# Optimization experiments

Hardware: AMD Instinct MI355X
Metric: run time of the kernel (lower is better)

Reference implementation:

```python
import jax, jax.numpy as jnp
import numpy as np

N_NODES = 50000
HIDDEN = 256
IN_DIM = 1000
OUT_DIM = 2
N_EDGES = 1600000


def gcn_conv(x, W, b, src, dst, n):
    # x: [N, Fin], W: [Fin, Fout]; src/dst already include self-loops
    h = x @ W  # [N, Fout]
    deg = jax.ops.segment_sum(jnp.ones(dst.shape, h.dtype), dst, num_segments=n)
    dinv = jnp.where(deg > 0, jax.lax.rsqrt(deg), 0.0)  # deg^{-1/2}
    norm = dinv[src] * dinv[dst]  # [E]
    out = jax.ops.segment_sum(h[src] * norm[:, None], dst, num_segments=n)
    return out + b


def setup_inputs() -> dict:
    key = jax.random.key(0)
    k1, k2, k3, k4 = jax.random.split(key, 4)
    x = jax.random.normal(k1, (N_NODES, IN_DIM), dtype=jnp.float32)
    edge_index = jax.random.randint(k2, (2, N_EDGES), 0, N_NODES, dtype=jnp.int64)
    # glorot-ish init for the two GCNConv layers
    W1 = jax.random.normal(k3, (IN_DIM, HIDDEN), dtype=jnp.float32) * (1.0 / np.sqrt(IN_DIM))
    b1 = jnp.zeros((HIDDEN,), dtype=jnp.float32)
    W2 = jax.random.normal(k4, (HIDDEN, OUT_DIM), dtype=jnp.float32) * (1.0 / np.sqrt(HIDDEN))
    b2 = jnp.zeros((OUT_DIM,), dtype=jnp.float32)
    return {"x": x, "W1": W1, "b1": b1, "W2": W2, "b2": b2, "edge_index": edge_index}


def reference(x, W1, b1, W2, b2, edge_index):
    n = x.shape[0]
    loops = jnp.arange(n, dtype=edge_index.dtype)
    src = jnp.concatenate([edge_index[0], loops])  # add self-loops (PyG gcn_norm)
    dst = jnp.concatenate([edge_index[1], loops])
    h = gcn_conv(x, W1, b1, src, dst, n)
    h = jax.nn.relu(h)
    out = gcn_conv(h, W2, b2, src, dst, n)
    return out
```

## Files before the change

### kernel.cpp

```cpp
#include <hip/hip_runtime.h>
#include <math.h>

#define N_NODES 50000
#define IN_DIM  1000
#define HIDDEN  256
#define N_EDGES 1600000
#define NBLK    196
#define NSTEP   63
#define GEMM_BLOCKS ((N_NODES + 63) / 64)
#define SCAT_BLOCKS 512

typedef short bf16x8 __attribute__((ext_vector_type(8)));
typedef float f32x16 __attribute__((ext_vector_type(16)));

__device__ __forceinline__ unsigned short f2bf_rne(float f) {
    unsigned u = __builtin_bit_cast(unsigned, f);
    unsigned r = (u + 0x7FFFu + ((u >> 16) & 1u)) >> 16;
    return (unsigned short)r;
}
__device__ __forceinline__ float bf2f(unsigned short b) {
    unsigned u = ((unsigned)b) << 16;
    return __builtin_bit_cast(float, u);
}
__device__ __forceinline__ unsigned cvt_pk_bf16(float a, float b) {
    unsigned r;
    asm("v_cvt_pk_bf16_f32 %0, %1, %2" : "=v"(r) : "v"(a), "v"(b));
    return r;
}
#define GLOAD_LDS16(gp, lp) \
    __builtin_amdgcn_global_load_lds((const __attribute__((address_space(1))) unsigned*)(gp), \
                                     (__attribute__((address_space(3))) unsigned*)(lp), 16, 0, 0)

__global__ void hist_kernel(const int* __restrict__ ei, int* __restrict__ cnt) {
    int e = blockIdx.x * blockDim.x + threadIdx.x;
    int stride = gridDim.x * blockDim.x;
    for (; e < N_EDGES; e += stride) {
        int d = ei[N_EDGES + e];
        if ((unsigned)d < N_NODES) atomicAdd(&cnt[d], 1);
    }
}

__global__ __launch_bounds__(256) void scan_sums(const int* __restrict__ cnt, int* __restrict__ bsum) {
    __shared__ int s[256];
    int t = threadIdx.x;
    int i = blockIdx.x * 256 + t;
    s[t] = (i < N_NODES) ? cnt[i] : 0;
    __syncthreads();
    #pragma unroll
    for (int off = 128; off > 0; off >>= 1) {
        if (t < off) s[t] += s[t + off];
        __syncthreads();
    }
    if (t == 0) bsum[blockIdx.x] = s[0];
}

__global__ __launch_bounds__(256) void scan_top(int* __restrict__ bsum) {
    __shared__ int s[256];
    int t = threadIdx.x;
    int v = (t < NBLK) ? bsum[t] : 0;
    s[t] = v;
    __syncthreads();
    for (int off = 1; off < 256; off <<= 1) {
        int x = (t >= off) ? s[t - off] : 0;
        __syncthreads();
        s[t] += x;
        __syncthreads();
    }
    if (t < NBLK) bsum[t] = s[t] - v;
}

__global__ __launch_bounds__(256) void scan_write(const int* __restrict__ cnt, const int* __restrict__ bsum,
                                                  int* __restrict__ rowoff, int* __restrict__ cursor,
                                                  float* __restrict__ dinv) {
    __shared__ int s[256];
    int t = threadIdx.x;
    int i = blockIdx.x * 256 + t;
    int v = (i < N_NODES) ? cnt[i] : 0;
    s[t] = v;
    __syncthreads();
    for (int off = 1; off < 256; off <<= 1) {
        int x = (t >= off) ? s[t - off] : 0;
        __syncthreads();
        s[t] += x;
        __syncthreads();
    }
    if (i < N_NODES) {
        int ro = bsum[blockIdx.x] + s[t] - v;
        rowoff[i] = ro;
        cursor[i] = ro;
        dinv[i]  = rsqrtf((float)v + 1.0f);
    }
}

__global__ __launch_bounds__(256) void wsplit_kernel(const float* __restrict__ W1,
                                                     unsigned short* __restrict__ Wp) {
    int idx = blockIdx.x * 256 + threadIdx.x;
    int c = idx >> 10, k = idx & 1023;
    float v = (k < IN_DIM) ? W1[(size_t)k * HIDDEN + c] : 0.0f;
    int ci = c >> 5;
    int step = k >> 4, kk = k & 15;
    int lane = (kk >> 3) * 32 + (c & 31);
    int j = kk & 7;
    Wp[((size_t)(step * 8 + ci) * 64 + lane) * 8 + j] = f2bf_rne(v);
}

__global__ __launch_bounds__(256, 4) void gemm_scatter_fused(const float* __restrict__ X,
                                                             const unsigned short* __restrict__ Wp,
                                                             const float* __restrict__ dinv,
                                                             unsigned short* __restrict__ G1b,
                                                             const int* __restrict__ ei,
                                                             int* __restrict__ cursor,
                                                             int* __restrict__ csr) {
    __shared__ unsigned short sA[2][1024];
    __shared__ unsigned short sB[2][4096];
    const int tid = threadIdx.x;

    if (blockIdx.x >= GEMM_BLOCKS) {
        int e = (blockIdx.x - GEMM_BLOCKS) * 256 + tid;
        int stride = SCAT_BLOCKS * 256;
        for (; e < N_EDGES; e += stride) {
            int s = ei[e];
            int d = ei[N_EDGES + e];
            if ((unsigned)d < N_NODES && (unsigned)s < N_NODES) {
                int pos = atomicAdd(&cursor[d], 1);
                csr[pos] = s;
            }
        }
        return;
    }

    const int w   = tid >> 6;
    const int l   = tid & 63;
    const int lr  = l & 31;
    const int lq  = l >> 5;
    const int R   = w >> 1;
    const int C   = w & 1;
    const int m0  = blockIdx.x * 64;

    const int rl = tid >> 2;
    const int ss = tid & 3;
    const int smt   = rl >> 5;
    const int slane = (ss >> 1) * 32 + (rl & 31);
    const int sidx  = smt * 512 + slane * 8 + (ss & 1) * 4;
    int rg = m0 + rl;
    const float* ap = X + (size_t)(rg < N_NODES ? rg : N_NODES - 1) * IN_DIM + ss * 4;
    const bool svalid_tail = (ss < 2);

    const unsigned short* bsrc = Wp + (size_t)(w * 2) * 512 + l * 8;

    f32x16 acc[4] = {};

    auto stageB = [&](int s, int buf) {
        const unsigned short* src = bsrc + (size_t)s * 4096;
        GLOAD_LDS16(src,       &sB[buf][(w * 2 + 0) * 512]);
        GLOAD_LDS16(src + 512, &sB[buf][(w * 2 + 1) * 512]);
    };
    auto cvtWriteA = [&](float4 f, int buf) {
        unsigned h0 = cvt_pk_bf16(f.x, f.y);
        unsigned h1 = cvt_pk_bf16(f.z, f.w);
        *(uint2*)&sA[buf][sidx] = make_uint2(h0, h1);
    };

    stageB(0, 0);
    cvtWriteA(*(const float4*)ap, 0);
    float4 rA = *(const float4*)(ap + 16);
    __syncthreads();

    #pragma unroll 1
    for (int s = 0; s < NSTEP; ++s) {
        const int buf = s & 1;
        if (s + 1 < NSTEP) stageB(s + 1, buf ^ 1);
        float4 rN = make_float4(0.f, 0.f, 0.f, 0.f);
        if (s + 2 < NSTEP && (s + 2 < NSTEP - 1 || svalid_tail))
            rN = *(const float4*)(ap + (size_t)(s + 2) * 16);
        if (s + 1 < NSTEP) cvtWriteA(rA, buf ^ 1);

        bf16x8 ah = *(const bf16x8*)&sA[buf][R * 512 + l * 8];
        bf16x8 b[4];
        #pragma unroll
        for (int ni = 0; ni < 4; ++ni)
            b[ni] = *(const bf16x8*)&sB[buf][(C * 4 + ni) * 512 + l * 8];
        #pragma unroll
        for (int ni = 0; ni < 4; ++ni)
            acc[ni] = __builtin_amdgcn_mfma_f32_32x32x16_bf16(ah, b[ni], acc[ni], 0, 0, 0);
        rA = rN;
        __syncthreads();
    }

    #pragma unroll
    for (int r = 0; r < 16; ++r) {
        int row = m0 + R * 32 + (r & 3) + 8 * (r >> 2) + 4 * lq;
        if (row >= N_NODES) continue;
        float dv = dinv[row];
        #pragma unroll
        for (int ni = 0; ni < 4; ++ni) {
            int slab = C * 4 + ni;
            G1b[((size_t)slab * N_NODES + row) * 32 + lr] = f2bf_rne(dv * acc[ni][r]);
        }
    }
}

__global__ __launch_bounds__(256) void aggslab_kernel(const unsigned short* __restrict__ G,
                                                      const int* __restrict__ csr,
                                                      const int* __restrict__ rowoff,
                                                      const int* __restrict__ cnt,
                                                      const float* __restrict__ dinv,
                                                      const float* __restrict__ b1,
                                                      const float* __restrict__ W2,
                                                      float* __restrict__ part) {
    const int tid  = threadIdx.x;
    const int slab = blockIdx.x & 7;
    const int nb   = blockIdx.x >> 3;
    const int wave = tid >> 6, lane = tid & 63;
    const int g    = lane >> 3, sl = lane & 7;
    const int d    = nb * 32 + wave * 8 + g;
    if (d >= N_NODES) return;
    const unsigned short* Gs = G + (size_t)slab * N_NODES * 32;
    const int co = sl * 4;
    const int c0 = slab * 32 + co;

    ushort4 sv = *(const ushort4*)&Gs[(size_t)d * 32 + co];
    float ax = bf2f(sv.x), ay = bf2f(sv.y), az = bf2f(sv.z), aw = bf2f(sv.w);
    int beg = rowoff[d], num = cnt[d];
    int end = beg + num;
    int e = beg;
    for (; e + 8 <= end; e += 8) {
        int s0 = csr[e], s1 = csr[e+1], s2 = csr[e+2], s3 = csr[e+3];
        int s4 = csr[e+4], s5 = csr[e+5], s6 = csr[e+6], s7 = csr[e+7];
        ushort4 v0 = *(const ushort4*)&Gs[(size_t)s0 * 32 + co];
        ushort4 v1 = *(const ushort4*)&Gs[(size_t)s1 * 32 + co];
        ushort4 v2 = *(const ushort4*)&Gs[(size_t)s2 * 32 + co];
        ushort4 v3 = *(const ushort4*)&Gs[(size_t)s3 * 32 + co];
        ushort4 v4 = *(const ushort4*)&Gs[(size_t)s4 * 32 + co];
        ushort4 v5 = *(const ushort4*)&Gs[(size_t)s5 * 32 + co];
        ushort4 v6 = *(const ushort4*)&Gs[(size_t)s6 * 32 + co];
        ushort4 v7 = *(const ushort4*)&Gs[(size_t)s7 * 32 + co];
        ax += bf2f(v0.x); ay += bf2f(v0.y); az += bf2f(v0.z); aw += bf2f(v0.w);
        ax += bf2f(v1.x); ay += bf2f(v1.y); az += bf2f(v1.z); aw += bf2f(v1.w);
        ax += bf2f(v2.x); ay += bf2f(v2.y); az += bf2f(v2.z); aw += bf2f(v2.w);
        ax += bf2f(v3.x); ay += bf2f(v3.y); az += bf2f(v3.z); aw += bf2f(v3.w);
        ax += bf2f(v4.x); ay += bf2f(v4.y); az += bf2f(v4.z); aw += bf2f(v4.w);
        ax += bf2f(v5.x); ay += bf2f(v5.y); az += bf2f(v5.z); aw += bf2f(v5.w);
        ax += bf2f(v6.x); ay += bf2f(v6.y); az += bf2f(v6.z); aw += bf2f(v6.w);
        ax += bf2f(v7.x); ay += bf2f(v7.y); az += bf2f(v7.z); aw += bf2f(v7.w);
    }
    for (; e < end; ++e) {
        int s = csr[e];
        ushort4 v = *(const ushort4*)&Gs[(size_t)s * 32 + co];
        ax += bf2f(v.x); ay += bf2f(v.y); az += bf2f(v.z); aw += bf2f(v.w);
    }
    float dv = dinv[d];
    float4 bb = *(const float4*)&b1[c0];
    float zx = fmaxf(dv * ax + bb.x, 0.f);
    float zy = fmaxf(dv * ay + bb.y, 0.f);
    float zz = fmaxf(dv * az + bb.z, 0.f);
    float zw = fmaxf(dv * aw + bb.w, 0.f);
    float2 w0 = *(const float2*)&W2[(c0 + 0) * 2];
    float2 w1 = *(const float2*)&W2[(c0 + 1) * 2];
    float2 w2_ = *(const float2*)&W2[(c0 + 2) * 2];
    float2 w3 = *(const float2*)&W2[(c0 + 3) * 2];
    float p0 = zx * w0.x + zy * w1.x + zz * w2_.x + zw * w3.x;
    float p1 = zx * w0.y + zy * w1.y + zz * w2_.y + zw * w3.y;
    #pragma unroll
    for (int off = 1; off < 8; off <<= 1) {
        p0 += __shfl_xor(p0, off, 64);
        p1 += __shfl_xor(p1, off, 64);
    }
    if (sl == 0)
        *(float2*)&part[((size_t)slab * N_NODES + d) * 2] = make_float2(p0, p1);
}

__global__ __launch_bounds__(256) void g2reduce_kernel(const float* __restrict__ part,
                                                       const float* __restrict__ dinv,
                                                       float* __restrict__ G2) {
    int i = blockIdx.x * 256 + threadIdx.x;
    if (i >= N_NODES) return;
    float a0 = 0.f, a1 = 0.f;
    #pragma unroll
    for (int s = 0; s < 8; ++s) {
        float2 p = *(const float2*)&part[((size_t)s * N_NODES + i) * 2];
        a0 += p.x; a1 += p.y;
    }
    float dv = dinv[i];
    G2[i * 2 + 0] = dv * a0;
    G2[i * 2 + 1] = dv * a1;
}

__global__ __launch_bounds__(256) void agg2_kernel(const float* __restrict__ G2,
                                                   const int* __restrict__ csr,
                                                   const int* __restrict__ rowoff,
                                                   const int* __restrict__ cnt,
                                                   const float* __restrict__ dinv,
                                                   const float* __restrict__ b2,
                                                   float* __restrict__ out) {
    int wave = threadIdx.x >> 6, lane = threadIdx.x & 63;
    int d = blockIdx.x * 4 + wave;
    if (d >= N_NODES) return;
    int beg = rowoff[d], num = cnt[d];
    float a0 = 0.f, a1 = 0.f;
    for (int e = lane; e < num; e += 64) {
        int s = csr[beg + e];
        float2 g = *(const float2*)&G2[s * 2];
        a0 += g.x; a1 += g.y;
    }
    #pragma unroll
    for (int off = 32; off; off >>= 1) {
        a0 += __shfl_xor(a0, off, 64);
        a1 += __shfl_xor(a1, off, 64);
    }
    if (lane == 0) {
        float2 self = *(const float2*)&G2[d * 2];
        float dv = dinv[d];
        out[d * 2 + 0] = dv * (a0 + self.x) + b2[0];
        out[d * 2 + 1] = dv * (a1 + self.y) + b2[1];
    }
}

#define OFF_CNT     0u
#define OFF_ROWOFF  262144u
#define OFF_CURSOR  524288u
#define OFF_DINV    786432u
#define OFF_BSUM    1048576u
#define OFF_CSR     1310720u
#define OFF_WP      8388608u
#define OFF_G1B     9437184u
#define OFF_G2      35651584u
#define OFF_PART    36700160u

extern "C" void kernel_launch(void* const* d_in, const int* in_sizes, int n_in,
                              void* d_out, int out_size, void* d_ws, size_t ws_size,
                              hipStream_t stream) {
    const float* x  = (const float*)d_in[0];
    const float* W1 = (const float*)d_in[1];
    const float* b1 = (const float*)d_in[2];
    const float* W2 = (const float*)d_in[3];
    const float* b2 = (const float*)d_in[4];
    const int*   ei = (const int*)d_in[5];

    char* ws = (char*)d_ws;
    int*   cnt    = (int*)  (ws + OFF_CNT);
    int*   rowoff = (int*)  (ws + OFF_ROWOFF);
    int*   cursor = (int*)  (ws + OFF_CURSOR);
    float* dinv   = (float*)(ws + OFF_DINV);
    int*   bsum   = (int*)  (ws + OFF_BSUM);
    int*   csr    = (int*)  (ws + OFF_CSR);
    unsigned short* wp  = (unsigned short*)(ws + OFF_WP);
    unsigned short* g1b = (unsigned short*)(ws + OFF_G1B);
    float* g2     = (float*)(ws + OFF_G2);
    float* part   = (float*)(ws + OFF_PART);
    float* out    = (float*)d_out;

    hipMemsetAsync(cnt, 0, N_NODES * sizeof(int), stream);
    wsplit_kernel<<<1024, 256, 0, stream>>>(W1, wp);
    hist_kernel<<<2048, 256, 0, stream>>>(ei, cnt);
    scan_sums<<<NBLK, 256, 0, stream>>>(cnt, bsum);
    scan_top<<<1, 256, 0, stream>>>(bsum);
    scan_write<<<NBLK, 256, 0, stream>>>(cnt, bsum, rowoff, cursor, dinv);

    gemm_scatter_fused<<<GEMM_BLOCKS + SCAT_BLOCKS, 256, 0, stream>>>(x, wp, dinv, g1b,
                                                                      ei, cursor, csr);

    aggslab_kernel<<<8 * ((N_NODES + 31) / 32), 256, 0, stream>>>(g1b, csr, rowoff, cnt, dinv, b1, W2, part);
    g2reduce_kernel<<<NBLK, 256, 0, stream>>>(part, dinv, g2);
    agg2_kernel<<<(N_NODES + 3) / 4, 256, 0, stream>>>(g2, csr, rowoff, cnt, dinv, b2, out);
}
```

Measured before the change: 297.3 us.

## Fuse prep kernels, partition CSR scatter by node range, replace slab reduce with atomics

Merges the W1 repack and degree histogram into one launch. The CSR scatter blocks are split into 8 groups that each handle only destinations in one node range, which localizes the cursor atomics and csr writes at the cost of each group re-reading the dst array. The separate g2 reduction kernel is dropped: aggslab atomically accumulates its partial results into a zeroed buffer, and agg2 applies dinv of each source itself. This saves a launch and the partial-buffer round trip, but adds float atomics with nondeterministic summation order and one extra memset.

```diff
diff --git a/kernel.cpp b/kernel.cpp
--- a/kernel.cpp
+++ b/kernel.cpp
@@ -9,6 +9,7 @@
 #define NSTEP   63
 #define GEMM_BLOCKS ((N_NODES + 63) / 64)
 #define SCAT_BLOCKS 512
+#define NODES_PER_PART 6250
 
 typedef short bf16x8 __attribute__((ext_vector_type(8)));
 typedef float f32x16 __attribute__((ext_vector_type(16)));
@@ -31,9 +32,24 @@
     __builtin_amdgcn_global_load_lds((const __attribute__((address_space(1))) unsigned*)(gp), \
                                      (__attribute__((address_space(3))) unsigned*)(lp), 16, 0, 0)
 
-__global__ void hist_kernel(const int* __restrict__ ei, int* __restrict__ cnt) {
-    int e = blockIdx.x * blockDim.x + threadIdx.x;
-    int stride = gridDim.x * blockDim.x;
+__global__ __launch_bounds__(256) void prep_kernel(const float* __restrict__ W1,
+                                                   unsigned short* __restrict__ Wp,
+                                                   const int* __restrict__ ei,
+                                                   int* __restrict__ cnt) {
+    const int tid = threadIdx.x;
+    if (blockIdx.x < 1024) {
+        int idx = blockIdx.x * 256 + tid;
+        int c = idx >> 10, k = idx & 1023;
+        float v = (k < IN_DIM) ? W1[(size_t)k * HIDDEN + c] : 0.0f;
+        int ci = c >> 5;
+        int step = k >> 4, kk = k & 15;
+        int lane = (kk >> 3) * 32 + (c & 31);
+        int j = kk & 7;
+        Wp[((size_t)(step * 8 + ci) * 64 + lane) * 8 + j] = f2bf_rne(v);
+        return;
+    }
+    int e = (blockIdx.x - 1024) * 256 + tid;
+    const int stride = 2048 * 256;
     for (; e < N_EDGES; e += stride) {
         int d = ei[N_EDGES + e];
         if ((unsigned)d < N_NODES) atomicAdd(&cnt[d], 1);
@@ -92,18 +108,6 @@
     }
 }
 
-__global__ __launch_bounds__(256) void wsplit_kernel(const float* __restrict__ W1,
-                                                     unsigned short* __restrict__ Wp) {
-    int idx = blockIdx.x * 256 + threadIdx.x;
-    int c = idx >> 10, k = idx & 1023;
-    float v = (k < IN_DIM) ? W1[(size_t)k * HIDDEN + c] : 0.0f;
-    int ci = c >> 5;
-    int step = k >> 4, kk = k & 15;
-    int lane = (kk >> 3) * 32 + (c & 31);
-    int j = kk & 7;
-    Wp[((size_t)(step * 8 + ci) * 64 + lane) * 8 + j] = f2bf_rne(v);
-}
-
 __global__ __launch_bounds__(256, 4) void gemm_scatter_fused(const float* __restrict__ X,
                                                              const unsigned short* __restrict__ Wp,
                                                              const float* __restrict__ dinv,
@@ -116,14 +120,21 @@
     const int tid = threadIdx.x;
 
     if (blockIdx.x >= GEMM_BLOCKS) {
-        int e = (blockIdx.x - GEMM_BLOCKS) * 256 + tid;
-        int stride = SCAT_BLOCKS * 256;
+        const int sb   = blockIdx.x - GEMM_BLOCKS;
+        const int part = blockIdx.x & 7;
+        const int q    = sb >> 3;
+        const int lo   = part * NODES_PER_PART;
+        const int hi   = lo + NODES_PER_PART;
+        int e = q * 256 + tid;
+        const int stride = (SCAT_BLOCKS / 8) * 256;
         for (; e < N_EDGES; e += stride) {
-            int s = ei[e];
             int d = ei[N_EDGES + e];
-            if ((unsigned)d < N_NODES && (unsigned)s < N_NODES) {
-                int pos = atomicAdd(&cursor[d], 1);
-                csr[pos] = s;
+            if (d >= lo && d < hi) {
+                int s = ei[e];
+                if ((unsigned)s < N_NODES) {
+                    int pos = atomicAdd(&cursor[d], 1);
+                    csr[pos] = s;
+                }
             }
         }
         return;
@@ -207,7 +218,7 @@
                                                       const float* __restrict__ dinv,
                                                       const float* __restrict__ b1,
                                                       const float* __restrict__ W2,
-                                                      float* __restrict__ part) {
+                                                      float* __restrict__ g2raw) {
     const int tid  = threadIdx.x;
     const int slab = blockIdx.x & 7;
     const int nb   = blockIdx.x >> 3;
@@ -266,27 +277,13 @@
         p0 += __shfl_xor(p0, off, 64);
         p1 += __shfl_xor(p1, off, 64);
     }
-    if (sl == 0)
-        *(float2*)&part[((size_t)slab * N_NODES + d) * 2] = make_float2(p0, p1);
-}
-
-__global__ __launch_bounds__(256) void g2reduce_kernel(const float* __restrict__ part,
-                                                       const float* __restrict__ dinv,
-                                                       float* __restrict__ G2) {
-    int i = blockIdx.x * 256 + threadIdx.x;
-    if (i >= N_NODES) return;
-    float a0 = 0.f, a1 = 0.f;
-    #pragma unroll
-    for (int s = 0; s < 8; ++s) {
-        float2 p = *(const float2*)&part[((size_t)s * N_NODES + i) * 2];
-        a0 += p.x; a1 += p.y;
-    }
-    float dv = dinv[i];
-    G2[i * 2 + 0] = dv * a0;
-    G2[i * 2 + 1] = dv * a1;
-}
-
-__global__ __launch_bounds__(256) void agg2_kernel(const float* __restrict__ G2,
+    if (sl == 0) {
+        atomicAdd(&g2raw[d * 2 + 0], p0);
+        atomicAdd(&g2raw[d * 2 + 1], p1);
+    }
+}
+
+__global__ __launch_bounds__(256) void agg2_kernel(const float* __restrict__ g2raw,
                                                    const int* __restrict__ csr,
                                                    const int* __restrict__ rowoff,
                                                    const int* __restrict__ cnt,
@@ -300,8 +297,9 @@
     float a0 = 0.f, a1 = 0.f;
     for (int e = lane; e < num; e += 64) {
         int s = csr[beg + e];
-        float2 g = *(const float2*)&G2[s * 2];
-        a0 += g.x; a1 += g.y;
+        float2 g = *(const float2*)&g2raw[s * 2];
+        float ds = dinv[s];
+        a0 += ds * g.x; a1 += ds * g.y;
     }
     #pragma unroll
     for (int off = 32; off; off >>= 1) {
@@ -309,10 +307,10 @@
         a1 += __shfl_xor(a1, off, 64);
     }
     if (lane == 0) {
-        float2 self = *(const float2*)&G2[d * 2];
+        float2 self = *(const float2*)&g2raw[d * 2];
         float dv = dinv[d];
-        out[d * 2 + 0] = dv * (a0 + self.x) + b2[0];
-        out[d * 2 + 1] = dv * (a1 + self.y) + b2[1];
+        out[d * 2 + 0] = dv * (a0 + dv * self.x) + b2[0];
+        out[d * 2 + 1] = dv * (a1 + dv * self.y) + b2[1];
     }
 }
 
@@ -325,7 +323,6 @@
 #define OFF_WP      8388608u
 #define OFF_G1B     9437184u
 #define OFF_G2      35651584u
-#define OFF_PART    36700160u
 
 extern "C" void kernel_launch(void* const* d_in, const int* in_sizes, int n_in,
                               void* d_out, int out_size, void* d_ws, size_t ws_size,
@@ -346,13 +343,13 @@
     int*   csr    = (int*)  (ws + OFF_CSR);
     unsigned short* wp  = (unsigned short*)(ws + OFF_WP);
     unsigned short* g1b = (unsigned short*)(ws + OFF_G1B);
-    float* g2     = (float*)(ws + OFF_G2);
-    float* part   = (float*)(ws + OFF_PART);
+    float* g2raw  = (float*)(ws + OFF_G2);
     float* out    = (float*)d_out;
 
     hipMemsetAsync(cnt, 0, N_NODES * sizeof(int), stream);
-    wsplit_kernel<<<1024, 256, 0, stream>>>(W1, wp);
-    hist_kernel<<<2048, 256, 0, stream>>>(ei, cnt);
+    hipMemsetAsync(g2raw, 0, N_NODES * 2 * sizeof(float), stream);
+
+    prep_kernel<<<3072, 256, 0, stream>>>(W1, wp, ei, cnt);
     scan_sums<<<NBLK, 256, 0, stream>>>(cnt, bsum);
     scan_top<<<1, 256, 0, stream>>>(bsum);
     scan_write<<<NBLK, 256, 0, stream>>>(cnt, bsum, rowoff, cursor, dinv);
@@ -360,7 +357,6 @@
     gemm_scatter_fused<<<GEMM_BLOCKS + SCAT_BLOCKS, 256, 0, stream>>>(x, wp, dinv, g1b,
                                                                       ei, cursor, csr);
 
-    aggslab_kernel<<<8 * ((N_NODES + 31) / 32), 256, 0, stream>>>(g1b, csr, rowoff, cnt, dinv, b1, W2, part);
-    g2reduce_kernel<<<NBLK, 256, 0, stream>>>(part, dinv, g2);
-    agg2_kernel<<<(N_NODES + 3) / 4, 256, 0, stream>>>(g2, csr, rowoff, cnt, dinv, b2, out);
-}
+    aggslab_kernel<<<8 * ((N_NODES + 31) / 32), 256, 0, stream>>>(g1b, csr, rowoff, cnt, dinv, b1, W2, g2raw);
+    agg2_kernel<<<(N_NODES + 3) / 4, 256, 0, stream>>>(g2raw, csr, rowoff, cnt, dinv, b2, out);
+}
```

New measurement: 365.5 us. +22.9%, slower.
